# Kernel optimization log

Measured on AMD Instinct MI355X. Metric: run time of the kernel, lower is better.

Reference implementation:

```python
import jax, jax.numpy as jnp
import numpy as np

# Production-scale dims
B, DZ, NW, NH, K = 8, 32, 48, 48, 25          # batch, dim_z, grid width/height, n_objects_max
W_RAW = H_RAW = 384.0                          # raw image size
SIZE_MIN, SIZE_MAX = 12.0, 48.0                # object size bounds
SCORE_T, OVER_T = 0.1, 0.3                     # score_threshold, overlap_threshold


def _conv1x1(x, w, b):
    # x: (B, d, nW, nH), w: (o, d), b: (o,) -> (B, o, nW, nH)  [Decoder1by1Linear]
    return jnp.einsum('bdwh,od->bowh', x, w) + b[None, :, None, None]


def _to_box_list(x):
    # (B, nW, nH) -> (N, B) with N = nW*nH, matching convert_to_box_list's permute(2,3,0,1).view
    return jnp.transpose(x, (1, 2, 0)).reshape(-1, x.shape[0])


def _nms(probT, x1, y1, x2, y2, k_max, score_t, over_t):
    # probT, x1..y2: (B, N). Greedy score/overlap NMS -> idx (B, K) int32, mask (B, N) float
    area = (x2 - x1) * (y2 - y1)
    xi1 = jnp.maximum(x1[:, :, None], x1[:, None, :])
    yi1 = jnp.maximum(y1[:, :, None], y1[:, None, :])
    xi2 = jnp.minimum(x2[:, :, None], x2[:, None, :])
    yi2 = jnp.minimum(y2[:, :, None], y2[:, None, :])
    inter = jnp.clip(xi2 - xi1, 0.0) * jnp.clip(yi2 - yi1, 0.0)
    union = area[:, :, None] + area[:, None, :] - inter
    iou = inter / jnp.maximum(union, 1e-8)                      # (B, N, N)
    possible0 = probT > score_t
    Bsz, N = probT.shape
    idx0 = jnp.zeros((Bsz, k_max), jnp.int32)
    val0 = jnp.zeros((Bsz, k_max), bool)

    def body(k, carry):
        possible, idxb, valb = carry
        masked = jnp.where(possible, probT, -jnp.inf)
        sel = jnp.argmax(masked, axis=1).astype(jnp.int32)      # (B,)
        ok = jnp.take_along_axis(possible, sel[:, None], axis=1)[:, 0]
        row = jnp.take_along_axis(iou, sel[:, None, None], axis=1)[:, 0, :]
        possible = possible & (row <= over_t)                   # suppresses sel itself (IoU=1)
        return possible, idxb.at[:, k].set(sel), valb.at[:, k].set(ok)

    _, idxb, valb = jax.lax.fori_loop(0, k_max, body, (possible0, idx0, val0))
    mask = jnp.zeros((Bsz, N), probT.dtype).at[jnp.arange(Bsz)[:, None], idxb].max(
        valb.astype(probT.dtype))
    return idxb, mask


def setup_inputs() -> dict:
    key = jax.random.key(0)
    ks = jax.random.split(key, 5)
    return {
        'zwhere_sample': jax.random.normal(ks[0], (B, DZ, NW, NH), jnp.float32),
        'w_zwhere': 0.2 * jax.random.normal(ks[1], (4, DZ), jnp.float32),
        'b_zwhere': jnp.zeros((4,), jnp.float32),
        'logit_sample': jax.random.normal(ks[2], (B, DZ, NW, NH), jnp.float32),
        'w_logit': 0.2 * jax.random.normal(ks[3], (1, DZ), jnp.float32),
        'b_logit': jnp.zeros((1,), jnp.float32),
        'weight_logits': jax.random.normal(ks[4], (K, B, 1, int(W_RAW), int(H_RAW)), jnp.float32),
    }


def reference(zwhere_sample, w_zwhere, b_zwhere, logit_sample, w_logit, b_logit, weight_logits):
    nW, nH = zwhere_sample.shape[-2:]
    # --- box decoding from zwhere latent map ---
    t = jax.nn.sigmoid(_conv1x1(zwhere_sample, w_zwhere, b_zwhere))  # (B,4,nW,nH)
    tx, ty, tw, th = t[:, 0], t[:, 1], t[:, 2], t[:, 3]
    ix = jnp.arange(nW, dtype=t.dtype)[:, None]   # ij meshgrid rows
    iy = jnp.arange(nH, dtype=t.dtype)[None, :]
    bx = W_RAW * (ix + tx) / nW
    by = H_RAW * (iy + ty) / nH
    bw = SIZE_MIN + (SIZE_MAX - SIZE_MIN) * tw
    bh = SIZE_MIN + (SIZE_MAX - SIZE_MIN) * th
    bx_l, by_l = _to_box_list(bx), _to_box_list(by)   # (N, B)
    bw_l, bh_l = _to_box_list(bw), _to_box_list(bh)
    # --- probability map from logit latent map ---
    p_map = jax.nn.sigmoid(_conv1x1(logit_sample, w_logit, b_logit))  # (B,1,nW,nH)
    prob_all = _to_box_list(p_map[:, 0])              # (N, B)
    probT = prob_all.T                                 # (B, N)
    x1 = (bx_l - 0.5 * bw_l).T
    x2 = (bx_l + 0.5 * bw_l).T
    y1 = (by_l - 0.5 * bh_l).T
    y2 = (by_l + 0.5 * bh_l).T
    # --- NMS under stop_gradient (torch.no_grad in original) ---
    sg = jax.lax.stop_gradient
    idxb, maskB = _nms(sg(probT), sg(x1), sg(y1), sg(x2), sg(y2), K, SCORE_T, OVER_T)
    # prob_few = gather(prob_all * nms_mask, index_top_k): differentiable w.r.t. prob_all
    prob_few = jnp.take_along_axis(probT * maskB, idxb, axis=1).T   # (K, B)
    # --- mask compositing (from_weights_to_masks over the object dim) ---
    big_weight = jax.nn.softplus(weight_logits)       # (K, B, 1, W, H)
    sum_w = jnp.sum(big_weight, axis=0, keepdims=True)
    big_mask = jnp.tanh(sum_w) * (big_weight / jnp.clip(sum_w, 1e-6))
    # probability-weighted masks (downstream compositing)
    return prob_few[:, :, None, None, None] * big_mask  # (K, B, 1, W, H)
```

## Files before the change

kernel.cpp:

```cpp
#include <hip/hip_runtime.h>
#include <math.h>

#define BATCH 8
#define DZ    32
#define NWH   48
#define NBOX  (NWH*NWH)
#define KMAX  25
#define PIX   (384*384)
#define NTHR  576
#define NW9   9

typedef float vfloat4 __attribute__((ext_vector_type(4)));

__device__ __forceinline__ float sigm(float x) { return 1.0f / (1.0f + expf(-x)); }
__device__ __forceinline__ float sp_fast(float x) {
    return fmaxf(x, 0.0f) + __logf(1.0f + __expf(-fabsf(x)));
}

__global__ __launch_bounds__(NTHR) void boxnms_kernel(
    const float* __restrict__ z, const float* __restrict__ wz, const float* __restrict__ bz,
    const float* __restrict__ lg, const float* __restrict__ wl, const float* __restrict__ bl,
    float* __restrict__ pfT)
{
    __shared__ vfloat4 boxS[NBOX];
    __shared__ float   prS[NBOX];
    __shared__ unsigned long long keyB[2][NW9];
    __shared__ int idxA[KMAX], okA[KMAX];

    const int b = blockIdx.x, t = threadIdx.x;
    const int iw = t / 12, ihq = t % 12;

    const float* zb = z  + (((size_t)b * DZ) * NWH + iw) * NWH + ihq * 4;
    const float* lb = lg + (((size_t)b * DZ) * NWH + iw) * NWH + ihq * 4;
    float b0 = bz[0], b1 = bz[1], b2 = bz[2], b3 = bz[3], blg = bl[0];
    vfloat4 a0 = {b0,b0,b0,b0}, a1 = {b1,b1,b1,b1}, a2 = {b2,b2,b2,b2},
            a3 = {b3,b3,b3,b3}, al = {blg,blg,blg,blg};
    #pragma unroll 8
    for (int d = 0; d < DZ; ++d) {
        vfloat4 zv = *(const vfloat4*)(zb + (size_t)d * NBOX);
        vfloat4 lv = *(const vfloat4*)(lb + (size_t)d * NBOX);
        float w0 = wz[d], w1 = wz[32+d], w2 = wz[64+d], w3 = wz[96+d], wv = wl[d];
        a0 += zv * w0; a1 += zv * w1; a2 += zv * w2; a3 += zv * w3; al += lv * wv;
    }

    float x1r[4], y1r[4], x2r[4], y2r[4], arr[4], mkv[4];
    int   nbs[4];
    {
        float t0v[4] = {a0.x,a0.y,a0.z,a0.w};
        float t1v[4] = {a1.x,a1.y,a1.z,a1.w};
        float t2v[4] = {a2.x,a2.y,a2.z,a2.w};
        float t3v[4] = {a3.x,a3.y,a3.z,a3.w};
        float alv[4] = {al.x,al.y,al.z,al.w};
        #pragma unroll
        for (int c = 0; c < 4; ++c) {
            float tx = sigm(t0v[c]), ty = sigm(t1v[c]), tw = sigm(t2v[c]), th = sigm(t3v[c]);
            float bx = 8.0f * ((float)iw + tx);
            float by = 8.0f * ((float)(ihq*4 + c) + ty);
            float bw = 12.0f + 36.0f * tw;
            float bh = 12.0f + 36.0f * th;
            float x1 = bx - 0.5f*bw, y1 = by - 0.5f*bh, x2 = bx + 0.5f*bw, y2 = by + 0.5f*bh;
            float p  = sigm(alv[c]);
            int   n  = iw * NWH + ihq*4 + c;
            x1r[c]=x1; y1r[c]=y1; x2r[c]=x2; y2r[c]=y2;
            arr[c] = (x2-x1)*(y2-y1);
            mkv[c] = (p > 0.1f) ? p : -INFINITY;
            nbs[c] = n;
            boxS[n] = (vfloat4){x1,y1,x2,y2};
            prS[n]  = p;
        }
    }

    float sx1=0.f, sy1=0.f, sx2=0.f, sy2=0.f, sar=0.f;
    for (int k = 0; k < KMAX; ++k) {
        unsigned long long best = 0ULL;
        #pragma unroll
        for (int c = 0; c < 4; ++c) {
            if (k > 0 && mkv[c] != -INFINITY) {
                float xi1 = fmaxf(sx1, x1r[c]);
                float yi1 = fmaxf(sy1, y1r[c]);
                float xi2 = fminf(sx2, x2r[c]);
                float yi2 = fminf(sy2, y2r[c]);
                float inter = fmaxf(xi2 - xi1, 0.f) * fmaxf(yi2 - yi1, 0.f);
                float uni   = sar + arr[c] - inter;
                float iou   = inter / fmaxf(uni, 1e-8f);
                if (iou > 0.3f) mkv[c] = -INFINITY;
            }
            if (mkv[c] != -INFINITY) {
                unsigned long long kk =
                    ((unsigned long long)__float_as_uint(mkv[c]) << 32) | (unsigned int)(~nbs[c]);
                if (kk > best) best = kk;
            }
        }
        #pragma unroll
        for (int off = 32; off > 0; off >>= 1) {
            unsigned long long o = __shfl_down(best, off);
            if (o > best) best = o;
        }
        if ((t & 63) == 0) keyB[k & 1][t >> 6] = best;
        __syncthreads();
        unsigned long long m = keyB[k & 1][0];
        #pragma unroll
        for (int w = 1; w < NW9; ++w) {
            unsigned long long o = keyB[k & 1][w];
            if (o > m) m = o;
        }
        int sel = (m == 0ULL) ? 0 : (int)(~(unsigned int)(m & 0xFFFFFFFFULL));
        if (t == 0) { idxA[k] = sel; okA[k] = (m != 0ULL); }
        vfloat4 sb = boxS[sel];
        sx1 = sb.x; sy1 = sb.y; sx2 = sb.z; sy2 = sb.w;
        sar = (sx2 - sx1) * (sy2 - sy1);
    }

    if (t == 0) {
        #pragma unroll 1
        for (int k = 0; k < KMAX; ++k) {
            float mm = 0.f;
            for (int k2 = 0; k2 < KMAX; ++k2)
                if (idxA[k2] == idxA[k] && okA[k2]) mm = 1.f;
            pfT[b * 32 + k] = prS[idxA[k]] * mm;
        }
    }
}

__global__ __launch_bounds__(256) void big_kernel(const float* __restrict__ wlg,
                                                  const float* __restrict__ pfT,
                                                  float* __restrict__ out)
{
    const size_t stride = (size_t)BATCH * PIX;
    const int b = (int)(((size_t)blockIdx.x * 1024) / PIX);
    const size_t j = ((size_t)blockIdx.x * 256 + threadIdx.x) * 4;
    const float* base = wlg + j;

    float sx = 0.f, sy = 0.f, sz = 0.f, sw = 0.f;
    #pragma unroll 5
    for (int k = 0; k < KMAX; ++k) {
        vfloat4 v = *(const vfloat4*)(base + (size_t)k * stride);
        sx += sp_fast(v.x); sy += sp_fast(v.y); sz += sp_fast(v.z); sw += sp_fast(v.w);
    }
    float mx, my, mz, mw;
    {
        float ex = __expf(-2.f*sx), ey = __expf(-2.f*sy), ez = __expf(-2.f*sz), ew = __expf(-2.f*sw);
        mx = (1.f - ex) * __builtin_amdgcn_rcpf(1.f + ex) * __builtin_amdgcn_rcpf(fmaxf(sx, 1e-6f));
        my = (1.f - ey) * __builtin_amdgcn_rcpf(1.f + ey) * __builtin_amdgcn_rcpf(fmaxf(sy, 1e-6f));
        mz = (1.f - ez) * __builtin_amdgcn_rcpf(1.f + ez) * __builtin_amdgcn_rcpf(fmaxf(sz, 1e-6f));
        mw = (1.f - ew) * __builtin_amdgcn_rcpf(1.f + ew) * __builtin_amdgcn_rcpf(fmaxf(sw, 1e-6f));
    }
    #pragma unroll 5
    for (int k = 0; k < KMAX; ++k) {
        vfloat4 v = *(const vfloat4*)(base + (size_t)k * stride);
        float c = pfT[b * 32 + k];
        vfloat4 o = { c * mx * sp_fast(v.x), c * my * sp_fast(v.y),
                      c * mz * sp_fast(v.z), c * mw * sp_fast(v.w) };
        __builtin_nontemporal_store(o, (vfloat4*)(out + (size_t)k * stride + j));
    }
}

extern "C" void kernel_launch(void* const* d_in, const int* in_sizes, int n_in,
                              void* d_out, int out_size, void* d_ws, size_t ws_size,
                              hipStream_t stream)
{
    const float* zwhere = (const float*)d_in[0];
    const float* w_zw   = (const float*)d_in[1];
    const float* b_zw   = (const float*)d_in[2];
    const float* logit  = (const float*)d_in[3];
    const float* w_lg   = (const float*)d_in[4];
    const float* b_lg   = (const float*)d_in[5];
    const float* wlogit = (const float*)d_in[6];
    float* out = (float*)d_out;
    float* pfT = (float*)d_ws;

    boxnms_kernel<<<BATCH, NTHR, 0, stream>>>(zwhere, w_zw, b_zw, logit, w_lg, b_lg, pfT);
    const int n4 = BATCH * PIX / 4;
    big_kernel<<<n4 / 256, 256, 0, stream>>>(wlogit, pfT, out);
}
```

Baseline: 110.9 us.

## Split object dim across 4 lanes and keep softplus in registers for single read

The compositing kernel now gives each group of 4 threads one float4 of pixels and splits the 25 object slices among them, 6 or 7 each. Partial softplus sums are combined with xor shuffles. The softplus values stay in registers, so the weight logits are read once instead of twice and the transcendental work is not redone. This roughly halves global read traffic and spreads the work over 4x more threads, at the cost of uneven load on lane 0 and some shuffle overhead.

```diff
diff --git a/kernel.cpp b/kernel.cpp
--- a/kernel.cpp
+++ b/kernel.cpp
@@ -127,31 +127,56 @@
                                                   float* __restrict__ out)
 {
     const size_t stride = (size_t)BATCH * PIX;
-    const int b = (int)(((size_t)blockIdx.x * 1024) / PIX);
-    const size_t j = ((size_t)blockIdx.x * 256 + threadIdx.x) * 4;
-    const float* base = wlg + j;
+    const int t = threadIdx.x;
+    const int r = t & 3;
+    const size_t j = ((size_t)blockIdx.x * 64 + (t >> 2)) * 4;
+    const int b = (int)(blockIdx.x / 576);
+    const int kb = 6 * r;
+    const float* base = wlg + (size_t)kb * stride + j;
 
-    float sx = 0.f, sy = 0.f, sz = 0.f, sw = 0.f;
-    #pragma unroll 5
-    for (int k = 0; k < KMAX; ++k) {
-        vfloat4 v = *(const vfloat4*)(base + (size_t)k * stride);
-        sx += sp_fast(v.x); sy += sp_fast(v.y); sz += sp_fast(v.z); sw += sp_fast(v.w);
+    vfloat4 acc = {0.f, 0.f, 0.f, 0.f};
+    vfloat4 sp0, sp1, sp2, sp3, sp4, sp5;
+#define LOADSP(s) { vfloat4 v = *(const vfloat4*)(base + (size_t)(s) * stride); \
+    sp##s = (vfloat4){ sp_fast(v.x), sp_fast(v.y), sp_fast(v.z), sp_fast(v.w) }; \
+    acc += sp##s; }
+    LOADSP(0) LOADSP(1) LOADSP(2) LOADSP(3) LOADSP(4) LOADSP(5)
+#undef LOADSP
+    vfloat4 sp6 = {0.f, 0.f, 0.f, 0.f};
+    if (r == 0) {
+        vfloat4 v = *(const vfloat4*)(wlg + (size_t)24 * stride + j);
+        sp6 = (vfloat4){ sp_fast(v.x), sp_fast(v.y), sp_fast(v.z), sp_fast(v.w) };
+        acc += sp6;
     }
-    float mx, my, mz, mw;
+
+    #pragma unroll
+    for (int mlane = 1; mlane <= 2; mlane <<= 1) {
+        acc.x += __shfl_xor(acc.x, mlane);
+        acc.y += __shfl_xor(acc.y, mlane);
+        acc.z += __shfl_xor(acc.z, mlane);
+        acc.w += __shfl_xor(acc.w, mlane);
+    }
+
+    vfloat4 m;
     {
-        float ex = __expf(-2.f*sx), ey = __expf(-2.f*sy), ez = __expf(-2.f*sz), ew = __expf(-2.f*sw);
-        mx = (1.f - ex) * __builtin_amdgcn_rcpf(1.f + ex) * __builtin_amdgcn_rcpf(fmaxf(sx, 1e-6f));
-        my = (1.f - ey) * __builtin_amdgcn_rcpf(1.f + ey) * __builtin_amdgcn_rcpf(fmaxf(sy, 1e-6f));
-        mz = (1.f - ez) * __builtin_amdgcn_rcpf(1.f + ez) * __builtin_amdgcn_rcpf(fmaxf(sz, 1e-6f));
-        mw = (1.f - ew) * __builtin_amdgcn_rcpf(1.f + ew) * __builtin_amdgcn_rcpf(fmaxf(sw, 1e-6f));
+        float ex = __expf(-2.f*acc.x), ey = __expf(-2.f*acc.y),
+              ez = __expf(-2.f*acc.z), ew = __expf(-2.f*acc.w);
+        m.x = (1.f - ex) * __builtin_amdgcn_rcpf(1.f + ex) * __builtin_amdgcn_rcpf(fmaxf(acc.x, 1e-6f));
+        m.y = (1.f - ey) * __builtin_amdgcn_rcpf(1.f + ey) * __builtin_amdgcn_rcpf(fmaxf(acc.y, 1e-6f));
+        m.z = (1.f - ez) * __builtin_amdgcn_rcpf(1.f + ez) * __builtin_amdgcn_rcpf(fmaxf(acc.z, 1e-6f));
+        m.w = (1.f - ew) * __builtin_amdgcn_rcpf(1.f + ew) * __builtin_amdgcn_rcpf(fmaxf(acc.w, 1e-6f));
     }
-    #pragma unroll 5
-    for (int k = 0; k < KMAX; ++k) {
-        vfloat4 v = *(const vfloat4*)(base + (size_t)k * stride);
-        float c = pfT[b * 32 + k];
-        vfloat4 o = { c * mx * sp_fast(v.x), c * my * sp_fast(v.y),
-                      c * mz * sp_fast(v.z), c * mw * sp_fast(v.w) };
-        __builtin_nontemporal_store(o, (vfloat4*)(out + (size_t)k * stride + j));
+
+    const float* pfb = pfT + b * 32 + kb;
+    float* ob = out + (size_t)kb * stride + j;
+#define STORE(s) { float c = pfb[s]; \
+    vfloat4 o = { c * m.x * sp##s.x, c * m.y * sp##s.y, c * m.z * sp##s.z, c * m.w * sp##s.w }; \
+    __builtin_nontemporal_store(o, (vfloat4*)(ob + (size_t)(s) * stride)); }
+    STORE(0) STORE(1) STORE(2) STORE(3) STORE(4) STORE(5)
+#undef STORE
+    if (r == 0) {
+        float c = pfT[b * 32 + 24];
+        vfloat4 o = { c * m.x * sp6.x, c * m.y * sp6.y, c * m.z * sp6.z, c * m.w * sp6.w };
+        __builtin_nontemporal_store(o, (vfloat4*)(out + (size_t)24 * stride + j));
     }
 }
 
@@ -170,6 +195,5 @@
     float* pfT = (float*)d_ws;
 
     boxnms_kernel<<<BATCH, NTHR, 0, stream>>>(zwhere, w_zw, b_zw, logit, w_lg, b_lg, pfT);
-    const int n4 = BATCH * PIX / 4;
-    big_kernel<<<n4 / 256, 256, 0, stream>>>(wlogit, pfT, out);
+    big_kernel<<<(BATCH * PIX) / 256, 256, 0, stream>>>(wlogit, pfT, out);
 }
```

Measured after the change: 94.28 us. 15.0% less time.
